# Kernel tuning notes

Hardware: AMD Instinct MI355X
Metric: run time of the kernel (lower is better)

Reference implementation:

```python
import jax, jax.numpy as jnp
import numpy as np
import math

B, S, D_EMB = 1, 4096, 768
N_HEADS, D_QKV = 12, 64
INV_TEMP = 1.0


def setup_inputs() -> dict:
    key = jax.random.key(0)
    ks = jax.random.split(key, 11)
    s = 0.02
    return {
        "q_in": jax.random.normal(ks[0], (B, S, D_EMB), jnp.float32),
        "k_in": jax.random.normal(ks[1], (B, S, D_EMB), jnp.float32),
        "v_in": jax.random.normal(ks[2], (B, S, D_EMB), jnp.float32),
        "W_q": jax.random.normal(ks[3], (D_EMB, N_HEADS * D_QKV), jnp.float32) * s,
        "b_q": jnp.zeros((N_HEADS * D_QKV,), jnp.float32),
        "W_k": jax.random.normal(ks[4], (D_EMB, N_HEADS * D_QKV), jnp.float32) * s,
        "b_k": jnp.zeros((N_HEADS * D_QKV,), jnp.float32),
        "W_v": jax.random.normal(ks[5], (D_EMB, N_HEADS * D_QKV), jnp.float32) * s,
        "b_v": jnp.zeros((N_HEADS * D_QKV,), jnp.float32),
        "W_o": jax.random.normal(ks[6], (N_HEADS * D_QKV, D_EMB), jnp.float32) * s,
        "b_o": jnp.zeros((D_EMB,), jnp.float32),
    }


def _split_heads(x):  # [B,S,H*D] -> [B,H,S,D]
    b, s, _ = x.shape
    return x.reshape(b, s, N_HEADS, D_QKV).transpose(0, 2, 1, 3)


def reference(q_in, k_in, v_in, W_q, b_q, W_k, b_k, W_v, b_v, W_o, b_o):
    q = _split_heads(q_in @ W_q + b_q)
    k = _split_heads(k_in @ W_k + b_k)
    v = _split_heads(v_in @ W_v + b_v)
    # full [B,H,S,S] score matrix (module materializes it for custom masking)
    scores = INV_TEMP * jnp.einsum('bhqd,bhkd->bhqk', q, k) / math.sqrt(D_QKV)
    attn = jax.nn.softmax(scores, axis=-1)
    out = jnp.einsum('bhqk,bhkd->bhqd', attn, v)  # [B,H,S,D]
    out = out.transpose(0, 2, 1, 3).reshape(q_in.shape[0], q_in.shape[1], N_HEADS * D_QKV)
    return out @ W_o + b_o
```

## Files before the change

kernel.cpp:

```cpp
#include <hip/hip_runtime.h>

#define S 4096
#define E 768
#define NH 12
#define DH 64
#define QSCALE (0.125f * 1.44269504f)
#define KSPLIT 4

typedef __bf16 bf16;
typedef __bf16 bf16x4 __attribute__((ext_vector_type(4)));
typedef __bf16 bf16x8 __attribute__((ext_vector_type(8)));
typedef float  f32x4  __attribute__((ext_vector_type(4)));

__device__ __forceinline__ void async16(const bf16* g, bf16* l) {
  __builtin_amdgcn_global_load_lds(
      (const __attribute__((address_space(1))) void*)g,
      (__attribute__((address_space(3))) void*)l, 16, 0, 0);
}

__global__ __launch_bounds__(256) void cast3(const float* __restrict__ i0,
                                             const float* __restrict__ i1,
                                             const float* __restrict__ i2,
                                             bf16* __restrict__ o0,
                                             bf16* __restrict__ o1,
                                             bf16* __restrict__ o2) {
  const float* in = blockIdx.z == 0 ? i0 : (blockIdx.z == 1 ? i1 : i2);
  bf16* out = blockIdx.z == 0 ? o0 : (blockIdx.z == 1 ? o1 : o2);
  int i = (blockIdx.x * blockDim.x + threadIdx.x) * 4;
  float4 v = *(const float4*)(in + i);
  bf16x4 o = { (bf16)v.x, (bf16)v.y, (bf16)v.z, (bf16)v.w };
  *(bf16x4*)(out + i) = o;
}

__global__ __launch_bounds__(256) void transpose4(const float* __restrict__ w0,
                                                  const float* __restrict__ w1,
                                                  const float* __restrict__ w2,
                                                  const float* __restrict__ w3,
                                                  bf16* __restrict__ t0,
                                                  bf16* __restrict__ t1,
                                                  bf16* __restrict__ t2,
                                                  bf16* __restrict__ t3) {
  const float* W = blockIdx.z == 0 ? w0 : (blockIdx.z == 1 ? w1 : (blockIdx.z == 2 ? w2 : w3));
  bf16* Wt = blockIdx.z == 0 ? t0 : (blockIdx.z == 1 ? t1 : (blockIdx.z == 2 ? t2 : t3));
  __shared__ float t[32][33];
  const int tx = threadIdx.x, ty = threadIdx.y;
  const int x = blockIdx.x * 32 + tx;
  const int y0 = blockIdx.y * 32;
  for (int j = ty; j < 32; j += 8)
    t[j][tx] = W[(y0 + j) * E + x];
  __syncthreads();
  for (int j = ty; j < 32; j += 8)
    Wt[(blockIdx.x * 32 + j) * E + y0 + tx] = (bf16)t[tx][j];
}

__global__ __launch_bounds__(256) void gemm128(const bf16* __restrict__ A0,
                                               const bf16* __restrict__ A1,
                                               const bf16* __restrict__ A2,
                                               const bf16* __restrict__ B0,
                                               const bf16* __restrict__ B1,
                                               const bf16* __restrict__ B2,
                                               const float* __restrict__ bias0,
                                               const float* __restrict__ bias1,
                                               const float* __restrict__ bias2,
                                               bf16* __restrict__ C0,
                                               bf16* __restrict__ C1,
                                               bf16* __restrict__ C2) {
  __shared__ __align__(16) bf16 smem[128 * 136];
  bf16* Asm = smem;
  bf16* Bsm = smem + 4096;
  bf16* Cs  = smem;

  const int z = blockIdx.z;
  const bf16* A  = z == 0 ? A0 : (z == 1 ? A1 : A2);
  const bf16* Bt = z == 0 ? B0 : (z == 1 ? B1 : B2);
  const float* bias = z == 0 ? bias0 : (z == 1 ? bias1 : bias2);

  const int tid = threadIdx.x;
  const int wv = tid >> 6, lane = tid & 63;
  const int quad = lane >> 4, l16 = lane & 15;
  const int m0 = blockIdx.x * 128, n0 = blockIdx.y * 128;
  const int wm = (wv >> 1) * 64, wn = (wv & 1) * 64;
  const int srow = lane >> 2, scol = (lane & 3) * 8;

  f32x4 acc[4][4] = {};

  for (int k0 = 0; k0 < E; k0 += 32) {
#pragma unroll
    for (int j = 0; j < 2; j++) {
      const int ch = wv * 2 + j;
      async16(&A[(size_t)(m0 + ch * 16 + srow) * E + k0 + scol], &Asm[ch * 512]);
      async16(&Bt[(size_t)(n0 + ch * 16 + srow) * E + k0 + scol], &Bsm[ch * 512]);
    }
    __syncthreads();
    bf16x8 af[4], bfv[4];
#pragma unroll
    for (int mi = 0; mi < 4; mi++)
      af[mi] = *(const bf16x8*)&Asm[(wm + mi * 16 + l16) * 32 + quad * 8];
#pragma unroll
    for (int ni = 0; ni < 4; ni++)
      bfv[ni] = *(const bf16x8*)&Bsm[(wn + ni * 16 + l16) * 32 + quad * 8];
#pragma unroll
    for (int mi = 0; mi < 4; mi++)
#pragma unroll
      for (int ni = 0; ni < 4; ni++)
        acc[mi][ni] = __builtin_amdgcn_mfma_f32_16x16x32_bf16(af[mi], bfv[ni], acc[mi][ni], 0, 0, 0);
    __syncthreads();
  }

  const float scale = (z == 0) ? QSCALE : 1.0f;
#pragma unroll
  for (int mi = 0; mi < 4; mi++) {
#pragma unroll
    for (int ni = 0; ni < 4; ni++) {
      const int nl = wn + ni * 16 + l16;
      const float bv = bias[n0 + nl];
#pragma unroll
      for (int r = 0; r < 4; r++) {
        const int ml = wm + mi * 16 + quad * 4 + r;
        const float v = (acc[mi][ni][r] + bv) * scale;
        if (z == 2) Cs[nl * 136 + ml] = (bf16)v;
        else        Cs[ml * 136 + nl] = (bf16)v;
      }
    }
  }
  __syncthreads();

  if (z == 0) {
    const int e = lane & 7;
#pragma unroll
    for (int p = 0; p < 8; p++) {
      const int hr = p * 32 + wv * 8 + (lane >> 3);
      const int r = hr >> 1, hf = hr & 1;
      bf16x8 c = *(const bf16x8*)&Cs[r * 136 + hf * 64 + e * 8];
      *(bf16x8*)(C0 + (size_t)((n0 >> 6) + hf) * S * DH + (size_t)(m0 + r) * DH + e * 8) = c;
    }
  } else {
    bf16* dst = (z == 1) ? C1 : C2;
    const int quadc = lane >> 4, l16c = lane & 15;
#pragma unroll
    for (int p = 0; p < 8; p++) {
      const int cid = p * 4 + wv;
      const int reg = cid >> 3;
      const int i = cid & 7;
      const int h_l = reg >> 1, tile = reg & 1;
      bf16x8 c;
      if (z == 1) {
        const int row = tile * 64 + (i >> 1) * 16 + l16c;
        const int col = h_l * 64 + (i & 1) * 32 + quadc * 8;
        c = *(const bf16x8*)&Cs[row * 136 + col];
      } else {
        const int nl = h_l * 64 + (i >> 1) * 16 + l16c;
        const int ml = tile * 64 + (i & 1) * 32 + quadc * 8;
        c = *(const bf16x8*)&Cs[nl * 136 + ml];
      }
      *(bf16x8*)(dst + (size_t)((n0 >> 6) + h_l) * S * DH +
                 (size_t)((m0 >> 6) + tile) * 4096 + i * 512 + lane * 8) = c;
    }
  }
}

__global__ __launch_bounds__(256, 4) void attn(const bf16* __restrict__ Q,
                                               const bf16* __restrict__ Kf,
                                               const bf16* __restrict__ Vf,
                                               bf16* __restrict__ Op0,
                                               bf16* __restrict__ Op1,
                                               bf16* __restrict__ Op2,
                                               bf16* __restrict__ Op3,
                                               float* __restrict__ Lp) {
  __shared__ bf16 P[4][32][76];
  const int h = blockIdx.y, ks = blockIdx.z;
  const int tid = threadIdx.x;
  const int wave = tid >> 6, lane = tid & 63;
  const int quad = lane >> 4, l16 = lane & 15;
  const int q0 = blockIdx.x * 128 + wave * 32;

  const bf16* Qh  = Q  + (size_t)h * S * DH;
  const bf16* Kfh = Kf + (size_t)h * S * DH;
  const bf16* Vfh = Vf + (size_t)h * S * DH;
  bf16* Op = ks == 0 ? Op0 : (ks == 1 ? Op1 : (ks == 2 ? Op2 : Op3));

  bf16x8 aq[2][2];
#pragma unroll
  for (int mi = 0; mi < 2; mi++)
#pragma unroll
    for (int j = 0; j < 2; j++)
      aq[mi][j] = *(const bf16x8*)&Qh[(size_t)(q0 + mi * 16 + l16) * DH + j * 32 + quad * 8];

  bf16x8 ones;
#pragma unroll
  for (int e = 0; e < 8; e++) ones[e] = (bf16)1.0f;

  f32x4 o[4][2] = {};
  f32x4 ol[2] = {};

  const bf16* kptr = Kfh + (size_t)ks * (S / KSPLIT) * DH + lane * 8;
  const bf16* vptr = Vfh + (size_t)ks * (S / KSPLIT) * DH + lane * 8;

  for (int it = 0; it < S / KSPLIT / 64; ++it, kptr += 4096, vptr += 4096) {
    bf16x8 kr[8];
#pragma unroll
    for (int i = 0; i < 8; i++) kr[i] = *(const bf16x8*)(kptr + i * 512);

#pragma unroll
    for (int mi = 0; mi < 2; mi++) {
      f32x4 sfr[4] = {};
#pragma unroll
      for (int nb = 0; nb < 4; nb++) {
        sfr[nb] = __builtin_amdgcn_mfma_f32_16x16x32_bf16(aq[mi][0], kr[nb * 2], sfr[nb], 0, 0, 0);
        sfr[nb] = __builtin_amdgcn_mfma_f32_16x16x32_bf16(aq[mi][1], kr[nb * 2 + 1], sfr[nb], 0, 0, 0);
      }
#pragma unroll
      for (int nb = 0; nb < 4; nb++)
#pragma unroll
        for (int r = 0; r < 4; r++)
          P[wave][mi * 16 + quad * 4 + r][nb * 16 + l16] = (bf16)__builtin_exp2f(sfr[nb][r]);
    }

    bf16x8 vr[8];
#pragma unroll
    for (int i = 0; i < 8; i++) vr[i] = *(const bf16x8*)(vptr + i * 512);

    bf16x8 ap[2][2];
#pragma unroll
    for (int mi = 0; mi < 2; mi++)
#pragma unroll
      for (int j = 0; j < 2; j++)
        ap[mi][j] = *(const bf16x8*)&P[wave][mi * 16 + l16][j * 32 + quad * 8];

#pragma unroll
    for (int mi = 0; mi < 2; mi++) {
      ol[mi] = __builtin_amdgcn_mfma_f32_16x16x32_bf16(ap[mi][0], ones, ol[mi], 0, 0, 0);
      ol[mi] = __builtin_amdgcn_mfma_f32_16x16x32_bf16(ap[mi][1], ones, ol[mi], 0, 0, 0);
    }
#pragma unroll
    for (int db = 0; db < 4; db++)
#pragma unroll
      for (int mi = 0; mi < 2; mi++) {
        o[db][mi] = __builtin_amdgcn_mfma_f32_16x16x32_bf16(ap[mi][0], vr[db * 2], o[db][mi], 0, 0, 0);
        o[db][mi] = __builtin_amdgcn_mfma_f32_16x16x32_bf16(ap[mi][1], vr[db * 2 + 1], o[db][mi], 0, 0, 0);
      }
  }

  float* Lph = Lp + (size_t)(ks * NH + h) * S;
  if (l16 == 0) {
#pragma unroll
    for (int mi = 0; mi < 2; mi++)
#pragma unroll
      for (int r = 0; r < 4; r++)
        Lph[q0 + mi * 16 + quad * 4 + r] = ol[mi][r];
  }
#pragma unroll
  for (int db = 0; db < 4; db++) {
    const int d = db * 16 + l16;
#pragma unroll
    for (int mi = 0; mi < 2; mi++)
#pragma unroll
      for (int r = 0; r < 4; r++) {
        const int row = q0 + mi * 16 + quad * 4 + r;
        Op[(size_t)row * E + h * DH + d] = (bf16)o[db][mi][r];
      }
  }
}

__global__ __launch_bounds__(256) void combine(const bf16* __restrict__ Op0,
                                               const bf16* __restrict__ Op1,
                                               const bf16* __restrict__ Op2,
                                               const bf16* __restrict__ Op3,
                                               const float* __restrict__ Lp,
                                               bf16* __restrict__ Obf) {
  const int i8 = blockIdx.x * 256 + threadIdx.x;
  const size_t base = (size_t)i8 * 8;
  const int row = (int)(base / E), c = (int)(base % E);
  const int h = c >> 6;
  const float l = Lp[(size_t)h * S + row] + Lp[(size_t)(NH + h) * S + row] +
                  Lp[(size_t)(2 * NH + h) * S + row] + Lp[(size_t)(3 * NH + h) * S + row];
  const float rl = 1.0f / l;
  bf16x8 a = *(const bf16x8*)(Op0 + base);
  bf16x8 b = *(const bf16x8*)(Op1 + base);
  bf16x8 cc = *(const bf16x8*)(Op2 + base);
  bf16x8 d = *(const bf16x8*)(Op3 + base);
  bf16x8 o;
#pragma unroll
  for (int e = 0; e < 8; e++)
    o[e] = (bf16)((((float)a[e] + (float)b[e]) + ((float)cc[e] + (float)d[e])) * rl);
  *(bf16x8*)(Obf + base) = o;
}

__global__ __launch_bounds__(256) void gemm64(const bf16* __restrict__ A,
                                              const bf16* __restrict__ Bt,
                                              const float* __restrict__ bias,
                                              float* __restrict__ C) {
  __shared__ __align__(16) bf16 Asm[64 * 32];
  __shared__ __align__(16) bf16 Bsm[64 * 32];
  const int tid = threadIdx.x;
  const int wv = tid >> 6, lane = tid & 63;
  const int quad = lane >> 4, l16 = lane & 15;
  const int m0 = blockIdx.x * 64, n0 = blockIdx.y * 64;
  const int srow = lane >> 2, scol = (lane & 3) * 8;

  f32x4 acc[4] = {};

  for (int k0 = 0; k0 < E; k0 += 32) {
    async16(&A[(size_t)(m0 + wv * 16 + srow) * E + k0 + scol], &Asm[wv * 512]);
    async16(&Bt[(size_t)(n0 + wv * 16 + srow) * E + k0 + scol], &Bsm[wv * 512]);
    __syncthreads();
    bf16x8 af = *(const bf16x8*)&Asm[(wv * 16 + l16) * 32 + quad * 8];
#pragma unroll
    for (int ni = 0; ni < 4; ni++) {
      bf16x8 bfr = *(const bf16x8*)&Bsm[(ni * 16 + l16) * 32 + quad * 8];
      acc[ni] = __builtin_amdgcn_mfma_f32_16x16x32_bf16(af, bfr, acc[ni], 0, 0, 0);
    }
    __syncthreads();
  }

  const int row0 = m0 + wv * 16 + quad * 4;
#pragma unroll
  for (int ni = 0; ni < 4; ni++) {
    const int col = n0 + ni * 16 + l16;
    const float bv = bias[col];
#pragma unroll
    for (int r = 0; r < 4; r++)
      C[(size_t)(row0 + r) * E + col] = acc[ni][r] + bv;
  }
}

extern "C" void kernel_launch(void* const* d_in, const int* in_sizes, int n_in,
                              void* d_out, int out_size, void* d_ws, size_t ws_size,
                              hipStream_t stream) {
  (void)in_sizes; (void)n_in; (void)out_size; (void)ws_size;
  const float* q_in = (const float*)d_in[0];
  const float* k_in = (const float*)d_in[1];
  const float* v_in = (const float*)d_in[2];
  const float* W_q  = (const float*)d_in[3];
  const float* b_q  = (const float*)d_in[4];
  const float* W_k  = (const float*)d_in[5];
  const float* b_k  = (const float*)d_in[6];
  const float* W_v  = (const float*)d_in[7];
  const float* b_v  = (const float*)d_in[8];
  const float* W_o  = (const float*)d_in[9];
  const float* b_o  = (const float*)d_in[10];

  const size_t SE2 = (size_t)S * E * 2;
  const size_t EE2 = (size_t)E * E * 2;
  char* ws = (char*)d_ws;
  bf16* qb  = (bf16*)(ws);
  bf16* kb  = (bf16*)(ws + SE2);
  bf16* vb  = (bf16*)(ws + 2 * SE2);
  bf16* WqT = (bf16*)(ws + 3 * SE2);
  bf16* WkT = (bf16*)(ws + 3 * SE2 + EE2);
  bf16* WvT = (bf16*)(ws + 3 * SE2 + 2 * EE2);
  bf16* WoT = (bf16*)(ws + 3 * SE2 + 3 * EE2);
  bf16* Qh  = (bf16*)(ws + 3 * SE2 + 4 * EE2);
  bf16* Kf  = (bf16*)(ws + 4 * SE2 + 4 * EE2);
  bf16* Vf  = (bf16*)(ws + 5 * SE2 + 4 * EE2);
  bf16* Obf = (bf16*)(ws + 6 * SE2 + 4 * EE2);
  bf16* Op1 = qb;
  bf16* Op2 = kb;
  bf16* Op3 = vb;
  float* Lp = (float*)WqT;

  cast3<<<dim3(S * E / 1024, 1, 3), 256, 0, stream>>>(q_in, k_in, v_in, qb, kb, vb);
  transpose4<<<dim3(24, 24, 4), dim3(32, 8), 0, stream>>>(W_q, W_k, W_v, W_o,
                                                          WqT, WkT, WvT, WoT);

  gemm128<<<dim3(S / 128, E / 128, 3), 256, 0, stream>>>(
      qb, kb, vb, WqT, WkT, WvT, b_q, b_k, b_v, Qh, Kf, Vf);

  attn<<<dim3(S / 128, NH, KSPLIT), 256, 0, stream>>>(Qh, Kf, Vf, Obf, Op1, Op2, Op3, Lp);

  combine<<<dim3(S * E / 2048), 256, 0, stream>>>(Obf, Op1, Op2, Op3, Lp, Obf);

  gemm64<<<dim3(S / 64, E / 64), 256, 0, stream>>>(Obf, WoT, b_o, (float*)d_out);
}
```

Before: 239.4 us.

## Stage K/V tiles through double-buffered LDS in attention, halve key split, merge prologue kernels

The attention kernel now has all four waves share each 64-key K/V tile. The tile is loaded cooperatively into a double-buffered LDS area with async global-to-LDS copies, so the next tile streams in while the current one is computed. Before, every wave read K and V straight from global memory into registers. The key-split factor drops from 4 to 2, which halves the partial outputs the combine kernel has to reduce but also halves the grid's parallelism, and the occupancy hint falls from 4 to 3 blocks per CU. The input cast and weight transpose kernels are merged into one launch to save a kernel launch.

```diff
diff --git a/kernel.cpp b/kernel.cpp
--- a/kernel.cpp
+++ b/kernel.cpp
@@ -5,52 +5,58 @@
 #define NH 12
 #define DH 64
 #define QSCALE (0.125f * 1.44269504f)
-#define KSPLIT 4
+#define KSPLIT 2
 
 typedef __bf16 bf16;
 typedef __bf16 bf16x4 __attribute__((ext_vector_type(4)));
 typedef __bf16 bf16x8 __attribute__((ext_vector_type(8)));
 typedef float  f32x4  __attribute__((ext_vector_type(4)));
 
+#define MFMA(a, b, c) __builtin_amdgcn_mfma_f32_16x16x32_bf16(a, b, c, 0, 0, 0)
+
 __device__ __forceinline__ void async16(const bf16* g, bf16* l) {
   __builtin_amdgcn_global_load_lds(
       (const __attribute__((address_space(1))) void*)g,
       (__attribute__((address_space(3))) void*)l, 16, 0, 0);
 }
 
-__global__ __launch_bounds__(256) void cast3(const float* __restrict__ i0,
-                                             const float* __restrict__ i1,
-                                             const float* __restrict__ i2,
-                                             bf16* __restrict__ o0,
-                                             bf16* __restrict__ o1,
-                                             bf16* __restrict__ o2) {
-  const float* in = blockIdx.z == 0 ? i0 : (blockIdx.z == 1 ? i1 : i2);
-  bf16* out = blockIdx.z == 0 ? o0 : (blockIdx.z == 1 ? o1 : o2);
-  int i = (blockIdx.x * blockDim.x + threadIdx.x) * 4;
-  float4 v = *(const float4*)(in + i);
-  bf16x4 o = { (bf16)v.x, (bf16)v.y, (bf16)v.z, (bf16)v.w };
-  *(bf16x4*)(out + i) = o;
-}
-
-__global__ __launch_bounds__(256) void transpose4(const float* __restrict__ w0,
-                                                  const float* __restrict__ w1,
-                                                  const float* __restrict__ w2,
-                                                  const float* __restrict__ w3,
-                                                  bf16* __restrict__ t0,
-                                                  bf16* __restrict__ t1,
-                                                  bf16* __restrict__ t2,
-                                                  bf16* __restrict__ t3) {
-  const float* W = blockIdx.z == 0 ? w0 : (blockIdx.z == 1 ? w1 : (blockIdx.z == 2 ? w2 : w3));
-  bf16* Wt = blockIdx.z == 0 ? t0 : (blockIdx.z == 1 ? t1 : (blockIdx.z == 2 ? t2 : t3));
-  __shared__ float t[32][33];
-  const int tx = threadIdx.x, ty = threadIdx.y;
-  const int x = blockIdx.x * 32 + tx;
-  const int y0 = blockIdx.y * 32;
-  for (int j = ty; j < 32; j += 8)
-    t[j][tx] = W[(y0 + j) * E + x];
-  __syncthreads();
-  for (int j = ty; j < 32; j += 8)
-    Wt[(blockIdx.x * 32 + j) * E + y0 + tx] = (bf16)t[tx][j];
+__global__ __launch_bounds__(256) void prologue(const float* __restrict__ q_in,
+                                                const float* __restrict__ k_in,
+                                                const float* __restrict__ v_in,
+                                                const float* __restrict__ w0,
+                                                const float* __restrict__ w1,
+                                                const float* __restrict__ w2,
+                                                const float* __restrict__ w3,
+                                                bf16* __restrict__ qb,
+                                                bf16* __restrict__ kb,
+                                                bf16* __restrict__ vb,
+                                                bf16* __restrict__ t0,
+                                                bf16* __restrict__ t1,
+                                                bf16* __restrict__ t2,
+                                                bf16* __restrict__ t3) {
+  const int bid = blockIdx.x, tid = threadIdx.x;
+  if (bid < 2304) {
+    const int z = bid / 576, rem = bid % 576;
+    const int bx = rem % 24, by = rem / 24;
+    const float* W = z == 0 ? w0 : (z == 1 ? w1 : (z == 2 ? w2 : w3));
+    bf16* Wt = z == 0 ? t0 : (z == 1 ? t1 : (z == 2 ? t2 : t3));
+    __shared__ float t[32][33];
+    const int tx = tid & 31, ty = tid >> 5;
+    for (int j = ty; j < 32; j += 8)
+      t[j][tx] = W[(by * 32 + j) * E + bx * 32 + tx];
+    __syncthreads();
+    for (int j = ty; j < 32; j += 8)
+      Wt[(bx * 32 + j) * E + by * 32 + tx] = (bf16)t[tx][j];
+  } else {
+    const int b2 = bid - 2304;
+    const int z = b2 / 3072, r2 = b2 % 3072;
+    const float* in = z == 0 ? q_in : (z == 1 ? k_in : v_in);
+    bf16* out = z == 0 ? qb : (z == 1 ? kb : vb);
+    const int i = r2 * 1024 + tid * 4;
+    float4 v = *(const float4*)(in + i);
+    bf16x4 o = { (bf16)v.x, (bf16)v.y, (bf16)v.z, (bf16)v.w };
+    *(bf16x4*)(out + i) = o;
+  }
 }
 
 __global__ __launch_bounds__(256) void gemm128(const bf16* __restrict__ A0,
@@ -103,7 +109,7 @@
     for (int mi = 0; mi < 4; mi++)
 #pragma unroll
       for (int ni = 0; ni < 4; ni++)
-        acc[mi][ni] = __builtin_amdgcn_mfma_f32_16x16x32_bf16(af[mi], bfv[ni], acc[mi][ni], 0, 0, 0);
+        acc[mi][ni] = MFMA(af[mi], bfv[ni], acc[mi][ni]);
     __syncthreads();
   }
 
@@ -136,7 +142,6 @@
     }
   } else {
     bf16* dst = (z == 1) ? C1 : C2;
-    const int quadc = lane >> 4, l16c = lane & 15;
 #pragma unroll
     for (int p = 0; p < 8; p++) {
       const int cid = p * 4 + wv;
@@ -145,12 +150,12 @@
       const int h_l = reg >> 1, tile = reg & 1;
       bf16x8 c;
       if (z == 1) {
-        const int row = tile * 64 + (i >> 1) * 16 + l16c;
-        const int col = h_l * 64 + (i & 1) * 32 + quadc * 8;
+        const int row = tile * 64 + (i >> 1) * 16 + l16;
+        const int col = h_l * 64 + (i & 1) * 32 + quad * 8;
         c = *(const bf16x8*)&Cs[row * 136 + col];
       } else {
-        const int nl = h_l * 64 + (i >> 1) * 16 + l16c;
-        const int ml = tile * 64 + (i & 1) * 32 + quadc * 8;
+        const int nl = h_l * 64 + (i >> 1) * 16 + l16;
+        const int ml = tile * 64 + (i & 1) * 32 + quad * 8;
         c = *(const bf16x8*)&Cs[nl * 136 + ml];
       }
       *(bf16x8*)(dst + (size_t)((n0 >> 6) + h_l) * S * DH +
@@ -159,14 +164,13 @@
   }
 }
 
-__global__ __launch_bounds__(256, 4) void attn(const bf16* __restrict__ Q,
+__global__ __launch_bounds__(256, 3) void attn(const bf16* __restrict__ Q,
                                                const bf16* __restrict__ Kf,
                                                const bf16* __restrict__ Vf,
                                                bf16* __restrict__ Op0,
                                                bf16* __restrict__ Op1,
-                                               bf16* __restrict__ Op2,
-                                               bf16* __restrict__ Op3,
                                                float* __restrict__ Lp) {
+  __shared__ __align__(16) bf16 KV[2][2][4096];
   __shared__ bf16 P[4][32][76];
   const int h = blockIdx.y, ks = blockIdx.z;
   const int tid = threadIdx.x;
@@ -174,10 +178,10 @@
   const int quad = lane >> 4, l16 = lane & 15;
   const int q0 = blockIdx.x * 128 + wave * 32;
 
-  const bf16* Qh  = Q  + (size_t)h * S * DH;
-  const bf16* Kfh = Kf + (size_t)h * S * DH;
-  const bf16* Vfh = Vf + (size_t)h * S * DH;
-  bf16* Op = ks == 0 ? Op0 : (ks == 1 ? Op1 : (ks == 2 ? Op2 : Op3));
+  const bf16* Qh  = Q + (size_t)h * S * DH;
+  const bf16* kt0 = Kf + (size_t)h * S * DH + (size_t)ks * (S / KSPLIT) * DH + lane * 8;
+  const bf16* vt0 = Vf + (size_t)h * S * DH + (size_t)ks * (S / KSPLIT) * DH + lane * 8;
+  bf16* Op = ks ? Op1 : Op0;
 
   bf16x8 aq[2][2];
 #pragma unroll
@@ -193,21 +197,37 @@
   f32x4 o[4][2] = {};
   f32x4 ol[2] = {};
 
-  const bf16* kptr = Kfh + (size_t)ks * (S / KSPLIT) * DH + lane * 8;
-  const bf16* vptr = Vfh + (size_t)ks * (S / KSPLIT) * DH + lane * 8;
-
-  for (int it = 0; it < S / KSPLIT / 64; ++it, kptr += 4096, vptr += 4096) {
+  const int f0 = wave * 2;
+#pragma unroll
+  for (int j = 0; j < 2; j++) {
+    async16(kt0 + (f0 + j) * 512, &KV[0][0][(f0 + j) * 512]);
+    async16(vt0 + (f0 + j) * 512, &KV[0][1][(f0 + j) * 512]);
+  }
+  __syncthreads();
+
+  const int T = S / KSPLIT / 64;
+  for (int t = 0; t < T; ++t) {
+    const int buf = t & 1;
+    if (t + 1 < T) {
+#pragma unroll
+      for (int j = 0; j < 2; j++) {
+        async16(kt0 + (size_t)(t + 1) * 4096 + (f0 + j) * 512, &KV[buf ^ 1][0][(f0 + j) * 512]);
+        async16(vt0 + (size_t)(t + 1) * 4096 + (f0 + j) * 512, &KV[buf ^ 1][1][(f0 + j) * 512]);
+      }
+    }
+
     bf16x8 kr[8];
 #pragma unroll
-    for (int i = 0; i < 8; i++) kr[i] = *(const bf16x8*)(kptr + i * 512);
+    for (int i = 0; i < 8; i++)
+      kr[i] = *(const bf16x8*)&KV[buf][0][i * 512 + lane * 8];
 
 #pragma unroll
     for (int mi = 0; mi < 2; mi++) {
       f32x4 sfr[4] = {};
 #pragma unroll
       for (int nb = 0; nb < 4; nb++) {
-        sfr[nb] = __builtin_amdgcn_mfma_f32_16x16x32_bf16(aq[mi][0], kr[nb * 2], sfr[nb], 0, 0, 0);
-        sfr[nb] = __builtin_amdgcn_mfma_f32_16x16x32_bf16(aq[mi][1], kr[nb * 2 + 1], sfr[nb], 0, 0, 0);
+        sfr[nb] = MFMA(aq[mi][0], kr[nb * 2], sfr[nb]);
+        sfr[nb] = MFMA(aq[mi][1], kr[nb * 2 + 1], sfr[nb]);
       }
 #pragma unroll
       for (int nb = 0; nb < 4; nb++)
@@ -216,10 +236,6 @@
           P[wave][mi * 16 + quad * 4 + r][nb * 16 + l16] = (bf16)__builtin_exp2f(sfr[nb][r]);
     }
 
-    bf16x8 vr[8];
-#pragma unroll
-    for (int i = 0; i < 8; i++) vr[i] = *(const bf16x8*)(vptr + i * 512);
-
     bf16x8 ap[2][2];
 #pragma unroll
     for (int mi = 0; mi < 2; mi++)
@@ -229,16 +245,21 @@
 
 #pragma unroll
     for (int mi = 0; mi < 2; mi++) {
-      ol[mi] = __builtin_amdgcn_mfma_f32_16x16x32_bf16(ap[mi][0], ones, ol[mi], 0, 0, 0);
-      ol[mi] = __builtin_amdgcn_mfma_f32_16x16x32_bf16(ap[mi][1], ones, ol[mi], 0, 0, 0);
-    }
-#pragma unroll
-    for (int db = 0; db < 4; db++)
+      ol[mi] = MFMA(ap[mi][0], ones, ol[mi]);
+      ol[mi] = MFMA(ap[mi][1], ones, ol[mi]);
+    }
+
+#pragma unroll
+    for (int db = 0; db < 4; db++) {
+      bf16x8 v0 = *(const bf16x8*)&KV[buf][1][(db * 2) * 512 + lane * 8];
+      bf16x8 v1 = *(const bf16x8*)&KV[buf][1][(db * 2 + 1) * 512 + lane * 8];
 #pragma unroll
       for (int mi = 0; mi < 2; mi++) {
-        o[db][mi] = __builtin_amdgcn_mfma_f32_16x16x32_bf16(ap[mi][0], vr[db * 2], o[db][mi], 0, 0, 0);
-        o[db][mi] = __builtin_amdgcn_mfma_f32_16x16x32_bf16(ap[mi][1], vr[db * 2 + 1], o[db][mi], 0, 0, 0);
-      }
+        o[db][mi] = MFMA(ap[mi][0], v0, o[db][mi]);
+        o[db][mi] = MFMA(ap[mi][1], v1, o[db][mi]);
+      }
+    }
+    __syncthreads();
   }
 
   float* Lph = Lp + (size_t)(ks * NH + h) * S;
@@ -264,25 +285,19 @@
 
 __global__ __launch_bounds__(256) void combine(const bf16* __restrict__ Op0,
                                                const bf16* __restrict__ Op1,
-                                               const bf16* __restrict__ Op2,
-                                               const bf16* __restrict__ Op3,
                                                const float* __restrict__ Lp,
                                                bf16* __restrict__ Obf) {
   const int i8 = blockIdx.x * 256 + threadIdx.x;
   const size_t base = (size_t)i8 * 8;
   const int row = (int)(base / E), c = (int)(base % E);
   const int h = c >> 6;
-  const float l = Lp[(size_t)h * S + row] + Lp[(size_t)(NH + h) * S + row] +
-                  Lp[(size_t)(2 * NH + h) * S + row] + Lp[(size_t)(3 * NH + h) * S + row];
+  const float l = Lp[(size_t)h * S + row] + Lp[(size_t)(NH + h) * S + row];
   const float rl = 1.0f / l;
   bf16x8 a = *(const bf16x8*)(Op0 + base);
   bf16x8 b = *(const bf16x8*)(Op1 + base);
-  bf16x8 cc = *(const bf16x8*)(Op2 + base);
-  bf16x8 d = *(const bf16x8*)(Op3 + base);
   bf16x8 o;
 #pragma unroll
-  for (int e = 0; e < 8; e++)
-    o[e] = (bf16)((((float)a[e] + (float)b[e]) + ((float)cc[e] + (float)d[e])) * rl);
+  for (int e = 0; e < 8; e++) o[e] = (bf16)(((float)a[e] + (float)b[e]) * rl);
   *(bf16x8*)(Obf + base) = o;
 }
 
@@ -308,7 +323,7 @@
 #pragma unroll
     for (int ni = 0; ni < 4; ni++) {
       bf16x8 bfr = *(const bf16x8*)&Bsm[(ni * 16 + l16) * 32 + quad * 8];
-      acc[ni] = __builtin_amdgcn_mfma_f32_16x16x32_bf16(af, bfr, acc[ni], 0, 0, 0);
+      acc[ni] = MFMA(af, bfr, acc[ni]);
     }
     __syncthreads();
   }
@@ -355,20 +370,17 @@
   bf16* Vf  = (bf16*)(ws + 5 * SE2 + 4 * EE2);
   bf16* Obf = (bf16*)(ws + 6 * SE2 + 4 * EE2);
   bf16* Op1 = qb;
-  bf16* Op2 = kb;
-  bf16* Op3 = vb;
   float* Lp = (float*)WqT;
 
-  cast3<<<dim3(S * E / 1024, 1, 3), 256, 0, stream>>>(q_in, k_in, v_in, qb, kb, vb);
-  transpose4<<<dim3(24, 24, 4), dim3(32, 8), 0, stream>>>(W_q, W_k, W_v, W_o,
-                                                          WqT, WkT, WvT, WoT);
+  prologue<<<dim3(2304 + 3 * 3072), 256, 0, stream>>>(
+      q_in, k_in, v_in, W_q, W_k, W_v, W_o, qb, kb, vb, WqT, WkT, WvT, WoT);
 
   gemm128<<<dim3(S / 128, E / 128, 3), 256, 0, stream>>>(
       qb, kb, vb, WqT, WkT, WvT, b_q, b_k, b_v, Qh, Kf, Vf);
 
-  attn<<<dim3(S / 128, NH, KSPLIT), 256, 0, stream>>>(Qh, Kf, Vf, Obf, Op1, Op2, Op3, Lp);
-
-  combine<<<dim3(S * E / 2048), 256, 0, stream>>>(Obf, Op1, Op2, Op3, Lp, Obf);
+  attn<<<dim3(S / 128, NH, KSPLIT), 256, 0, stream>>>(Qh, Kf, Vf, Obf, Op1, Lp);
+
+  combine<<<dim3(S * E / 2048), 256, 0, stream>>>(Obf, Op1, Lp, Obf);
 
   gemm64<<<dim3(S / 64, E / 64), 256, 0, stream>>>(Obf, WoT, b_o, (float*)d_out);
 }
```

After: 238.9 us. No clear change (-0.2%).
